# Performance work log

Measured on AMD Instinct MI355X. Metric: run time of the kernel, lower is better.

The kernel has to match this reference:

```python
import jax, jax.numpy as jnp
import numpy as np

D_MODEL = 1024
NHEAD = 16
HEAD_DIM = D_MODEL // NHEAD
D_FF = 4096
EPS = 1e-5


def _layernorm(x, g, b):
    mu = jnp.mean(x, axis=-1, keepdims=True)
    var = jnp.mean(jnp.square(x - mu), axis=-1, keepdims=True)
    return (x - mu) * jax.lax.rsqrt(var + EPS) * g + b


def setup_inputs() -> dict:
    key = jax.random.key(0)
    ks = jax.random.split(key, 8)

    def xavier(k, shape):
        fan_out, fan_in = shape
        lim = np.sqrt(6.0 / (fan_in + fan_out))
        return jax.random.uniform(k, shape, jnp.float32, -lim, lim)

    x = jax.random.normal(ks[0], (4, 2048, D_MODEL), jnp.float32)
    return {
        "x": x,
        "Wq": xavier(ks[1], (D_MODEL, D_MODEL)), "bq": jnp.zeros((D_MODEL,), jnp.float32),
        "Wk": xavier(ks[2], (D_MODEL, D_MODEL)), "bk": jnp.zeros((D_MODEL,), jnp.float32),
        "Wv": xavier(ks[3], (D_MODEL, D_MODEL)), "bv": jnp.zeros((D_MODEL,), jnp.float32),
        "Wo": xavier(ks[4], (D_MODEL, D_MODEL)), "bo": jnp.zeros((D_MODEL,), jnp.float32),
        "W1": xavier(ks[5], (D_FF, D_MODEL)), "b1": jnp.zeros((D_FF,), jnp.float32),
        "W2": xavier(ks[6], (D_MODEL, D_FF)), "b2": jnp.zeros((D_MODEL,), jnp.float32),
        "ln1_g": jnp.ones((D_MODEL,), jnp.float32), "ln1_b": jnp.zeros((D_MODEL,), jnp.float32),
        "ln2_g": jnp.ones((D_MODEL,), jnp.float32), "ln2_b": jnp.zeros((D_MODEL,), jnp.float32),
    }


def reference(x, Wq, bq, Wk, bk, Wv, bv, Wo, bo, W1, b1, W2, b2, ln1_g, ln1_b, ln2_g, ln2_b):
    B, T, D = x.shape
    H, Hd = NHEAD, HEAD_DIM

    # --- attention sublayer (pre-LN) ---
    residual = x
    xn = _layernorm(x, ln1_g, ln1_b)
    # torch Linear: y = x @ W.T + b
    q = (xn @ Wq.T + bq).reshape(B, T, H, Hd).transpose(0, 2, 1, 3)  # [B,H,T,Hd]
    k = (xn @ Wk.T + bk).reshape(B, T, H, Hd).transpose(0, 2, 1, 3)
    v = (xn @ Wv.T + bv).reshape(B, T, H, Hd).transpose(0, 2, 1, 3)

    scale = Hd ** -0.5
    scores = jnp.einsum('bhqd,bhkd->bhqk', q, k) * scale  # [B,H,T,T]
    attn = jax.nn.softmax(scores, axis=-1)
    out = jnp.einsum('bhqk,bhkd->bhqd', attn, v)           # [B,H,T,Hd]
    out = out.transpose(0, 2, 1, 3).reshape(B, T, D)
    out = out @ Wo.T + bo
    x = residual + out

    # --- FFN sublayer (pre-LN) ---
    residual = x
    xn = _layernorm(x, ln2_g, ln2_b)
    h = jax.nn.relu(xn @ W1.T + b1)
    h = h @ W2.T + b2
    return residual + h
```

## Files before the change

kernel.cpp:

```cpp
#include <hip/hip_runtime.h>
#include <hip/hip_bf16.h>

using bf16 = __hip_bfloat16;
typedef __attribute__((ext_vector_type(8))) short bf16x8;
typedef __attribute__((ext_vector_type(4))) float f32x4;

#define D_MODEL 1024
#define NHEAD 16
#define HEAD_DIM 64
#define D_FF 4096
#define SEQ 2048
#define NTOK 8192

__device__ __forceinline__ void gload16(const void* g, void* l) {
  __builtin_amdgcn_global_load_lds((const __attribute__((address_space(1))) void*)g,
                                   (__attribute__((address_space(3))) void*)l, 16, 0, 0);
}

__device__ __forceinline__ unsigned pkbf16(float lo, float hi) {
  unsigned r;
  asm("v_cvt_pk_bf16_f32 %0, %1, %2" : "=v"(r) : "v"(lo), "v"(hi));
  return r;
}

__device__ __forceinline__ float fexp2(float x) {
  float r;
  asm("v_exp_f32 %0, %1" : "=v"(r) : "v"(x));
  return r;
}

__device__ __forceinline__ float max3f(float a, float b, float c) {
  return fmaxf(fmaxf(a, b), c);
}

__global__ __launch_bounds__(256) void cvt_all(
    const float* __restrict__ W1, const float* __restrict__ W2,
    const float* __restrict__ Wq, const float* __restrict__ Wk,
    const float* __restrict__ Wv, const float* __restrict__ Wo,
    bf16* __restrict__ w1_b, bf16* __restrict__ w2_b,
    bf16* __restrict__ wqkv, bf16* __restrict__ wo_b) {
  const int bid = blockIdx.x;
  const float* src;
  bf16* dst;
  int lb;
  if (bid < 4096) { src = W1; dst = w1_b; lb = bid; }
  else if (bid < 8192) { src = W2; dst = w2_b; lb = bid - 4096; }
  else {
    const int j = (bid - 8192) >> 10;
    lb = (bid - 8192) & 1023;
    if (j == 0) { src = Wq; dst = wqkv; }
    else if (j == 1) { src = Wk; dst = wqkv + 1048576; }
    else if (j == 2) { src = Wv; dst = wqkv + 2097152; }
    else { src = Wo; dst = wo_b; }
  }
  const int i = (lb * 256 + threadIdx.x) * 4;
  const float4 v = *(const float4*)&src[i];
  dst[i + 0] = __float2bfloat16(v.x);
  dst[i + 1] = __float2bfloat16(v.y);
  dst[i + 2] = __float2bfloat16(v.z);
  dst[i + 3] = __float2bfloat16(v.w);
}

__global__ __launch_bounds__(256) void layernorm_kernel(
    const float* __restrict__ xin, const float* __restrict__ g,
    const float* __restrict__ bta, bf16* __restrict__ out) {
  const int row = blockIdx.x, t = threadIdx.x;
  const float4 v = *(const float4*)&xin[(size_t)row * D_MODEL + t * 4];
  float s = v.x + v.y + v.z + v.w;
#pragma unroll
  for (int m = 1; m < 64; m <<= 1) s += __shfl_xor(s, m);
  __shared__ float red[4], red2[4];
  const int w = t >> 6, l = t & 63;
  if (l == 0) red[w] = s;
  __syncthreads();
  const float mu = (red[0] + red[1] + red[2] + red[3]) * (1.f / 1024.f);
  const float d0 = v.x - mu, d1 = v.y - mu, d2 = v.z - mu, d3 = v.w - mu;
  float q = d0 * d0 + d1 * d1 + d2 * d2 + d3 * d3;
#pragma unroll
  for (int m = 1; m < 64; m <<= 1) q += __shfl_xor(q, m);
  if (l == 0) red2[w] = q;
  __syncthreads();
  const float var = (red2[0] + red2[1] + red2[2] + red2[3]) * (1.f / 1024.f);
  const float rs = rsqrtf(var + 1e-5f);
  const float4 gg = *(const float4*)&g[t * 4];
  const float4 bb = *(const float4*)&bta[t * 4];
  bf16* o = out + (size_t)row * D_MODEL + t * 4;
  o[0] = __float2bfloat16(d0 * rs * gg.x + bb.x);
  o[1] = __float2bfloat16(d1 * rs * gg.y + bb.y);
  o[2] = __float2bfloat16(d2 * rs * gg.z + bb.z);
  o[3] = __float2bfloat16(d3 * rs * gg.w + bb.w);
}

template <int MODE>
__global__ __launch_bounds__(512, 2) void gemmA(
    const bf16* __restrict__ A, const bf16* __restrict__ Bw,
    const float* __restrict__ bias0, const float* __restrict__ bias1,
    const float* __restrict__ bias2,
    void* __restrict__ out, int M, int N, int K) {
  constexpr int ASZ = 256 * 128;
  constexpr int TILE = ASZ + 256 * 128;
  __shared__ __align__(16) char smem[2 * TILE];

  const int t = threadIdx.x;
  const int l = t & 63, l15 = l & 15, l4 = (l >> 4) & 3;
  const int w = t >> 6, wm = w >> 2, wn = w & 3;
  const int gx = gridDim.x;
  const int nwg = gx * gridDim.y;
  const int bid0 = blockIdx.y * gx + blockIdx.x;
  const int bid = (bid0 & 7) * (nwg >> 3) + (bid0 >> 3);
  const int m0 = (bid / gx) * 256, n0 = (bid % gx) * 256;

  const int sr = t >> 3;
  const int scol = 8 * ((t & 7) ^ (sr & 7));
  const int swz = (l15 & 7) << 4;
  int coff[2];
  coff[0] = (l4 * 16) ^ swz;
  coff[1] = (64 + l4 * 16) ^ swz;

#define ST_A(j, kb, buf)                                          \
  gload16(&A[(size_t)(m0 + (j) * 64 + sr) * K + (kb) + scol],     \
          (void*)(smem + (buf) * TILE + (j) * 8192 + t * 16))
#define ST_B(j, kb, buf)                                          \
  gload16(&Bw[(size_t)(n0 + (j) * 64 + sr) * K + (kb) + scol],    \
          (void*)(smem + (buf) * TILE + ASZ + (j) * 8192 + t * 16))

  f32x4 acc[8][4] = {};
  const int NTm = K >> 6;

  ST_A(0, 0, 0); ST_A(2, 0, 0); ST_B(0, 0, 0);
  ST_B(1, 0, 0); ST_B(2, 0, 0); ST_B(3, 0, 0);
  ST_A(1, 0, 0); ST_A(3, 0, 0);
  asm volatile("s_waitcnt vmcnt(2)" ::: "memory");
  __builtin_amdgcn_s_barrier();

#define PHASE_A(p)                                                                 \
  {                                                                                \
    constexpr int kk = (p) & 1;                                                    \
    constexpr int mh = ((p) >> 1) * 4;                                             \
    bf16x8 af[4], bf[4];                                                           \
    _Pragma("unroll") for (int m = 0; m < 4; ++m)                                  \
      af[m] = *(const bf16x8*)(cb + (wm * 128 + (mh + m) * 16 + l15) * 128 +       \
                               coff[kk]);                                          \
    _Pragma("unroll") for (int n = 0; n < 4; ++n)                                  \
      bf[n] = *(const bf16x8*)(cb + ASZ + (wn * 64 + n * 16 + l15) * 128 +         \
                               coff[kk]);                                          \
    if (hasNext) {                                                                 \
      if ((p) == 0) { ST_A(0, kbn, nb); ST_A(2, kbn, nb); ST_B(0, kbn, nb); }      \
      else if ((p) == 1) { ST_B(1, kbn, nb); ST_B(2, kbn, nb); ST_B(3, kbn, nb); } \
      else if ((p) == 2) { ST_A(1, kbn, nb); ST_A(3, kbn, nb); }                   \
    }                                                                              \
    __builtin_amdgcn_s_barrier();                                                  \
    asm volatile("s_waitcnt lgkmcnt(0)" ::: "memory");                             \
    __builtin_amdgcn_sched_barrier(0);                                             \
    __builtin_amdgcn_s_setprio(1);                                                 \
    _Pragma("unroll") for (int m = 0; m < 4; ++m)                                  \
      _Pragma("unroll") for (int n = 0; n < 4; ++n)                                \
        acc[mh + m][n] = __builtin_amdgcn_mfma_f32_16x16x32_bf16(                  \
            af[m], bf[n], acc[mh + m][n], 0, 0, 0);                                \
    __builtin_amdgcn_s_setprio(0);                                                 \
    if ((p) == 1) {                                                                \
      if (hasNext) asm volatile("s_waitcnt vmcnt(6)" ::: "memory");                \
      else asm volatile("s_waitcnt vmcnt(0)" ::: "memory");                        \
    }                                                                              \
    if ((p) == 3 && hasNext)                                                       \
      asm volatile("s_waitcnt vmcnt(2)" ::: "memory");                             \
    __builtin_amdgcn_s_barrier();                                                  \
  }

  for (int kt = 0; kt < NTm; ++kt) {
    const char* cb = smem + (kt & 1) * TILE;
    const int nb = (kt & 1) ^ 1;
    const int kbn = (kt + 1) << 6;
    const bool hasNext = (kt + 1 < NTm);
    PHASE_A(0) PHASE_A(1) PHASE_A(2) PHASE_A(3)
  }
#undef PHASE_A
#undef ST_A
#undef ST_B

#pragma unroll
  for (int mf = 0; mf < 8; ++mf) {
#pragma unroll
    for (int nf = 0; nf < 4; ++nf) {
      const int col = n0 + wn * 64 + nf * 16 + l15;
      float bb;
      if constexpr (MODE == 0) {
        const int sel = col >> 10;
        const float* bp = (sel == 0) ? bias0 : ((sel == 1) ? bias1 : bias2);
        bb = bp[col & 1023];
      } else {
        bb = bias0[col];
      }
#pragma unroll
      for (int r = 0; r < 4; ++r) {
        const int row = m0 + wm * 128 + mf * 16 + l4 * 4 + r;
        float y = acc[mf][nf][r] + bb;
        if constexpr (MODE == 1) y = fmaxf(y, 0.f);
        if constexpr (MODE == 0) {
          const int sel = col >> 10;
          const int c10 = col & 1023;
          const size_t dst = (size_t)sel * (NTOK * 1024) +
                             (size_t)((row >> 11) * NHEAD + (c10 >> 6)) * (SEQ * HEAD_DIM) +
                             (size_t)(row & (SEQ - 1)) * HEAD_DIM + (c10 & 63);
          ((bf16*)out)[dst] = __float2bfloat16(y);
        } else {
          ((bf16*)out)[(size_t)row * N + col] = __float2bfloat16(y);
        }
      }
    }
  }
}

__global__ __launch_bounds__(512, 2) void gemmB(
    const bf16* __restrict__ A, const bf16* __restrict__ Bw,
    const float* __restrict__ bias, const float* __restrict__ res,
    float* __restrict__ out, int M, int N, int K) {
  constexpr int ASZ = 128 * 128;
  constexpr int TILE = ASZ + 256 * 128;
  __shared__ __align__(16) char smem[3 * TILE];

  const int t = threadIdx.x;
  const int l = t & 63, l15 = l & 15, l4 = (l >> 4) & 3;
  const int w = t >> 6, wm = w >> 2, wn = w & 3;
  const int gx = gridDim.x;
  const int nwg = gx * gridDim.y;
  const int bid0 = blockIdx.y * gx + blockIdx.x;
  const int bid = (bid0 & 7) * (nwg >> 3) + (bid0 >> 3);
  const int m0 = (bid / gx) * 128, n0 = (bid % gx) * 256;

  const int sr = t >> 3;
  const int scol = 8 * ((t & 7) ^ (sr & 7));
  const int swz = (l15 & 7) << 4;
  int coff[2];
  coff[0] = (l4 * 16) ^ swz;
  coff[1] = (64 + l4 * 16) ^ swz;

#define ST_A(j, kb, buf)                                          \
  gload16(&A[(size_t)(m0 + (j) * 64 + sr) * K + (kb) + scol],     \
          (void*)(smem + (buf) * TILE + (j) * 8192 + t * 16))
#define ST_B(j, kb, buf)                                          \
  gload16(&Bw[(size_t)(n0 + (j) * 64 + sr) * K + (kb) + scol],    \
          (void*)(smem + (buf) * TILE + ASZ + (j) * 8192 + t * 16))

  f32x4 acc[4][4] = {};
  const int NTm = K >> 6;

  ST_B(0, 0, 0); ST_B(1, 0, 0); ST_B(2, 0, 0);
  ST_B(3, 0, 0); ST_A(0, 0, 0); ST_A(1, 0, 0);
  ST_B(0, 64, 1); ST_B(1, 64, 1); ST_B(2, 64, 1);
  ST_B(3, 64, 1); ST_A(0, 64, 1); ST_A(1, 64, 1);
  asm volatile("s_waitcnt vmcnt(6)" ::: "memory");
  __builtin_amdgcn_s_barrier();

#define PHASE_B(p)                                                                 \
  {                                                                                \
    constexpr int kk = (p);                                                        \
    bf16x8 af[4], bf[4];                                                           \
    _Pragma("unroll") for (int m = 0; m < 4; ++m)                                  \
      af[m] = *(const bf16x8*)(cb + (wm * 64 + m * 16 + l15) * 128 + coff[kk]);    \
    _Pragma("unroll") for (int n = 0; n < 4; ++n)                                  \
      bf[n] = *(const bf16x8*)(cb + ASZ + (wn * 64 + n * 16 + l15) * 128 +         \
                               coff[kk]);                                          \
    if (iss) {                                                                     \
      if ((p) == 0) { ST_B(0, kbn, nb); ST_B(1, kbn, nb); ST_B(2, kbn, nb); }      \
      else { ST_B(3, kbn, nb); ST_A(0, kbn, nb); ST_A(1, kbn, nb); }               \
    }                                                                              \
    __builtin_amdgcn_s_barrier();                                                  \
    asm volatile("s_waitcnt lgkmcnt(0)" ::: "memory");                             \
    __builtin_amdgcn_sched_barrier(0);                                             \
    __builtin_amdgcn_s_setprio(1);                                                 \
    _Pragma("unroll") for (int m = 0; m < 4; ++m)                                  \
      _Pragma("unroll") for (int n = 0; n < 4; ++n)                                \
        acc[m][n] = __builtin_amdgcn_mfma_f32_16x16x32_bf16(                       \
            af[m], bf[n], acc[m][n], 0, 0, 0);                                     \
    __builtin_amdgcn_s_setprio(0);                                                 \
    if ((p) == 1) {                                                                \
      if (iss) asm volatile("s_waitcnt vmcnt(6)" ::: "memory");                    \
      else asm volatile("s_waitcnt vmcnt(0)" ::: "memory");                        \
    }                                                                              \
    __builtin_amdgcn_s_barrier();                                                  \
  }

  for (int kt = 0; kt < NTm; ++kt) {
    const char* cb = smem + (kt % 3) * TILE;
    const int nb = (kt + 2) % 3;
    const int kbn = (kt + 2) << 6;
    const bool iss = (kt + 2 < NTm);
    PHASE_B(0) PHASE_B(1)
  }
#undef PHASE_B
#undef ST_A
#undef ST_B

#pragma unroll
  for (int mf = 0; mf < 4; ++mf) {
#pragma unroll
    for (int nf = 0; nf < 4; ++nf) {
      const int col = n0 + wn * 64 + nf * 16 + l15;
      const float bb = bias[col];
#pragma unroll
      for (int r = 0; r < 4; ++r) {
        const int row = m0 + wm * 64 + mf * 16 + l4 * 4 + r;
        out[(size_t)row * N + col] = acc[mf][nf][r] + bb + res[(size_t)row * N + col];
      }
    }
  }
}

#define SCL 0.18033688011112042f
#define NT (SEQ / 64)

__global__ __launch_bounds__(512) void flash_attn(
    const bf16* __restrict__ Q, const bf16* __restrict__ K,
    const bf16* __restrict__ V, bf16* __restrict__ O) {
  __shared__ char smem[32768];
  const int t = threadIdx.x;
  const int w = t >> 6, l = t & 63;
  const int l15 = l & 15, l4 = l >> 4;
  const int bid0 = blockIdx.y * 8 + blockIdx.x;
  const int bid = (bid0 & 7) * 64 + (bid0 >> 3);
  const int bx = bid & 7, bh = bid >> 3;
  const size_t base = (size_t)bh * (SEQ * HEAD_DIM);
  const int q0 = bx * 256 + w * 32;

  int krow[4], kswz[4];
#pragma unroll
  for (int ni = 0; ni < 4; ++ni) {
    const int kr = (ni >> 1) * 32 + (ni & 1) * 4 + (l15 >> 2) * 8 + (l15 & 3);
    krow[ni] = kr * 128;
    kswz[ni] = ((kr & 3) | (((kr >> 3) & 1) << 2)) << 4;
  }

  bf16x8 qf[2][2];
#pragma unroll
  for (int mi = 0; mi < 2; ++mi)
#pragma unroll
    for (int kk = 0; kk < 2; ++kk)
      qf[mi][kk] = *(const bf16x8*)&Q[base + (size_t)(q0 + mi * 16 + l15) * 64 + kk * 32 + l4 * 8];

  bf16x8 ones;
#pragma unroll
  for (int j = 0; j < 8; ++j) ones[j] = (short)0x3F80;

  f32x4 accO[2][4] = {};
  float m_run[2], l_run[2];
#pragma unroll
  for (int mi = 0; mi < 2; ++mi) { m_run[mi] = -1e30f; l_run[mi] = 0.f; }

  short vg[8];

  const int r0 = t >> 3;
  const int c0 = 8 * ((t & 7) ^ ((r0 & 3) | (((r0 >> 3) & 1) << 2)));
  const short* kg = (const short*)K + base + r0 * 64 + c0;
  const int dv = t & 63;
  const int kb8 = (t >> 6) * 8;
  const short* vp = (const short*)V + base + (size_t)kb8 * 64 + dv;
  const int vtbyte = dv * 128 + ((kb8 * 2) ^ ((dv & 7) << 4));

#define STAGE_K(bufofs)                                          \
  {                                                              \
    gload16(kg, (void*)(smem + (bufofs) + w * 1024));            \
    kg += 4096;                                                  \
  }

#define V_GATHER()                                               \
  {                                                              \
    _Pragma("unroll") for (int j_ = 0; j_ < 8; ++j_)             \
        vg[j_] = vp[j_ * 64];                                    \
    vp += 4096;                                                  \
  }

#define VT_WRITE(bufofs)                                         \
  {                                                              \
    bf16x8 vv;                                                   \
    _Pragma("unroll") for (int j_ = 0; j_ < 8; ++j_)             \
        vv[j_] = vg[j_];                                         \
    *(bf16x8*)(smem + (bufofs) + vtbyte) = vv;                   \
  }

  STAGE_K(0);
  V_GATHER();
  VT_WRITE(16384);
  __syncthreads();

  for (int it = 0; it < NT; ++it) {
    const int cur = it & 1;
    const char* Kb = (const char*)smem + cur * 8192;
    const char* Vb = (const char*)smem + 16384 + cur * 8192;
    const bool pre = (it + 1 < NT);
    if (pre) {
      STAGE_K((cur ^ 1) * 8192);
      V_GATHER();
    }

    bf16x8 kf[2][4];
#pragma unroll
    for (int kk = 0; kk < 2; ++kk)
#pragma unroll
      for (int ni = 0; ni < 4; ++ni)
        kf[kk][ni] = *(const bf16x8*)(Kb + krow[ni] + ((kk * 64 + l4 * 16) ^ kswz[ni]));

    unsigned pw[2][8];
#pragma unroll
    for (int mi = 0; mi < 2; ++mi) {
      f32x4 s[4] = {};
      __builtin_amdgcn_s_setprio(1);
#pragma unroll
      for (int kk = 0; kk < 2; ++kk)
#pragma unroll
        for (int ni = 0; ni < 4; ++ni)
          s[ni] = __builtin_amdgcn_mfma_f32_16x16x32_bf16(kf[kk][ni], qf[mi][kk], s[ni], 0, 0, 0);
      __builtin_amdgcn_s_setprio(0);

      const float t0 = max3f(s[0][0], s[0][1], s[0][2]);
      const float t1 = max3f(s[0][3], s[1][0], s[1][1]);
      const float t2 = max3f(s[1][2], s[1][3], s[2][0]);
      const float t3 = max3f(s[2][1], s[2][2], s[2][3]);
      const float t4 = max3f(s[3][0], s[3][1], s[3][2]);
      float mx = fmaxf(max3f(t1, t2, t3), fmaxf(t4, fmaxf(t0, s[3][3])));
      mx = fmaxf(mx, __shfl_xor(mx, 16));
      mx = fmaxf(mx, __shfl_xor(mx, 32));
      const float mxs = mx * SCL;
      if (__any(mxs > m_run[mi] + 8.f)) {
        const float mn = fmaxf(m_run[mi], mxs);
        const float c = fexp2(m_run[mi] - mn);
        m_run[mi] = mn;
        l_run[mi] *= c;
#pragma unroll
        for (int ni = 0; ni < 4; ++ni)
#pragma unroll
          for (int r = 0; r < 4; ++r) accO[mi][ni][r] *= c;
      }
#pragma unroll
      for (int ni = 0; ni < 4; ++ni)
#pragma unroll
        for (int r = 0; r < 4; ++r)
          s[ni][r] = fexp2(fmaf(s[ni][r], SCL, -m_run[mi]));
#pragma unroll
      for (int kk = 0; kk < 2; ++kk)
#pragma unroll
        for (int jj = 0; jj < 4; ++jj) {
          const int ni = 2 * kk + (jj >> 1);
          pw[mi][kk * 4 + jj] = pkbf16(s[ni][2 * (jj & 1)], s[ni][2 * (jj & 1) + 1]);
        }
    }

    f32x4 zz[2] = {};
#pragma unroll
    for (int kk = 0; kk < 2; ++kk) {
      bf16x8 vf[4];
#pragma unroll
      for (int ni = 0; ni < 4; ++ni)
        vf[ni] = *(const bf16x8*)(Vb + (ni * 16 + l15) * 128 +
                                  ((kk * 64 + l4 * 16) ^ ((l15 & 7) << 4)));
#pragma unroll
      for (int mi = 0; mi < 2; ++mi) {
        union { unsigned u[4]; bf16x8 h; } pb;
#pragma unroll
        for (int jj = 0; jj < 4; ++jj) pb.u[jj] = pw[mi][kk * 4 + jj];
        __builtin_amdgcn_s_setprio(1);
#pragma unroll
        for (int ni = 0; ni < 4; ++ni)
          accO[mi][ni] = __builtin_amdgcn_mfma_f32_16x16x32_bf16(vf[ni], pb.h, accO[mi][ni], 0, 0, 0);
        zz[mi] = __builtin_amdgcn_mfma_f32_16x16x32_bf16(ones, pb.h, zz[mi], 0, 0, 0);
        __builtin_amdgcn_s_setprio(0);
      }
    }
#pragma unroll
    for (int mi = 0; mi < 2; ++mi) l_run[mi] += zz[mi][0];

    if (pre) VT_WRITE(16384 + (cur ^ 1) * 8192);
    __syncthreads();
  }

  char* ob = smem + w * 4096;
#pragma unroll
  for (int mi = 0; mi < 2; ++mi) {
    const float inv = 1.f / l_run[mi];
    const int qr = mi * 16 + l15;
    const int sw = (qr & 7) << 4;
#pragma unroll
    for (int ni = 0; ni < 4; ++ni)
#pragma unroll
      for (int rr = 0; rr < 2; ++rr) {
        const unsigned pk = pkbf16(accO[mi][ni][2 * rr] * inv, accO[mi][ni][2 * rr + 1] * inv);
        *(unsigned*)(ob + qr * 128 + ((ni * 32 + l4 * 8 + 4 * rr) ^ sw)) = pk;
      }
  }
  asm volatile("s_waitcnt lgkmcnt(0)" ::: "memory");
  __builtin_amdgcn_sched_barrier(0);

  const int b = bh >> 4, h = bh & 15;
  const int hr = l >> 1, hf = l & 1;
  const size_t orow = ((size_t)b * SEQ + bx * 256 + w * 32 + hr) * D_MODEL + h * HEAD_DIM + hf * 32;
#pragma unroll
  for (int c = 0; c < 4; ++c) {
    bf16x8 vv = *(const bf16x8*)(ob + hr * 128 + (((hf * 64) + c * 16) ^ ((hr & 7) << 4)));
    *(bf16x8*)&O[orow + c * 8] = vv;
  }
}

extern "C" void kernel_launch(void* const* d_in, const int* in_sizes, int n_in,
                              void* d_out, int out_size, void* d_ws, size_t ws_size,
                              hipStream_t stream) {
  const float* x     = (const float*)d_in[0];
  const float* Wq    = (const float*)d_in[1];
  const float* bq    = (const float*)d_in[2];
  const float* Wk    = (const float*)d_in[3];
  const float* bk    = (const float*)d_in[4];
  const float* Wv    = (const float*)d_in[5];
  const float* bv    = (const float*)d_in[6];
  const float* Wo    = (const float*)d_in[7];
  const float* bo    = (const float*)d_in[8];
  const float* W1    = (const float*)d_in[9];
  const float* b1    = (const float*)d_in[10];
  const float* W2    = (const float*)d_in[11];
  const float* b2    = (const float*)d_in[12];
  const float* ln1_g = (const float*)d_in[13];
  const float* ln1_b = (const float*)d_in[14];
  const float* ln2_g = (const float*)d_in[15];
  const float* ln2_b = (const float*)d_in[16];

  const size_t MB = 1ull << 20;
  char* ws = (char*)d_ws;
  bf16* wqkv = (bf16*)(ws + 0 * MB);
  bf16* wo_b = (bf16*)(ws + 6 * MB);
  bf16* w1_b = (bf16*)(ws + 8 * MB);
  bf16* w2_b = (bf16*)(ws + 16 * MB);
  bf16* xn   = (bf16*)(ws + 24 * MB);
  bf16* qb   = (bf16*)(ws + 40 * MB);
  bf16* kbuf = (bf16*)(ws + 56 * MB);
  bf16* vb   = (bf16*)(ws + 72 * MB);
  bf16* hb   = (bf16*)(ws + 40 * MB);
  float* x1  = (float*)(ws + 104 * MB);

  cvt_all<<<12288, 256, 0, stream>>>(W1, W2, Wq, Wk, Wv, Wo, w1_b, w2_b, wqkv, wo_b);

  layernorm_kernel<<<NTOK, 256, 0, stream>>>(x, ln1_g, ln1_b, xn);

  gemmA<0><<<dim3(3072 / 256, NTOK / 256), 512, 0, stream>>>(
      xn, wqkv, bq, bk, bv, qb, NTOK, 3072, 1024);

  flash_attn<<<dim3(SEQ / 256, 4 * NHEAD), 512, 0, stream>>>(qb, kbuf, vb, xn);

  gemmB<<<dim3(1024 / 256, NTOK / 128), 512, 0, stream>>>(
      xn, wo_b, bo, x, x1, NTOK, 1024, 1024);

  layernorm_kernel<<<NTOK, 256, 0, stream>>>(x1, ln2_g, ln2_b, xn);

  gemmA<1><<<dim3(D_FF / 256, NTOK / 256), 512, 0, stream>>>(
      xn, w1_b, b1, b1, b1, hb, NTOK, D_FF, 1024);

  gemmB<<<dim3(1024 / 256, NTOK / 128), 512, 0, stream>>>(
      hb, w2_b, b2, x1, (float*)d_out, NTOK, 1024, D_FF);
}
```

Baseline: 384.4 us.

## Simplify GEMM pipelines and move QKV projection onto 128-row triple-buffered kernel

Both GEMM kernels drop the fine-grained four-phase and two-phase schedules, which interleaved async loads with barriers and partial vmcnt waits. The new loops issue each tile's loads up front, read all fragments, run the MFMAs, then do one wait and one barrier per k-step. The QKV projection moves from the 256x256 double-buffered kernel to the 128x256 triple-buffered kernel, now templated to handle the head-split scatter output. gemmA keeps only the FFN1 path and now waits on vmcnt(0) every iteration, which may expose load latency. The changes aim to cut barrier and sync overhead and to raise the QKV grid size, at the cost of less overlap between loads and compute.

```diff
diff --git a/kernel.cpp b/kernel.cpp
--- a/kernel.cpp
+++ b/kernel.cpp
@@ -94,8 +94,7 @@
 template <int MODE>
 __global__ __launch_bounds__(512, 2) void gemmA(
     const bf16* __restrict__ A, const bf16* __restrict__ Bw,
-    const float* __restrict__ bias0, const float* __restrict__ bias1,
-    const float* __restrict__ bias2,
+    const float* __restrict__ bias0,
     void* __restrict__ out, int M, int N, int K) {
   constexpr int ASZ = 256 * 128;
   constexpr int TILE = ASZ + 256 * 128;
@@ -127,59 +126,142 @@
   f32x4 acc[8][4] = {};
   const int NTm = K >> 6;
 
-  ST_A(0, 0, 0); ST_A(2, 0, 0); ST_B(0, 0, 0);
-  ST_B(1, 0, 0); ST_B(2, 0, 0); ST_B(3, 0, 0);
-  ST_A(1, 0, 0); ST_A(3, 0, 0);
-  asm volatile("s_waitcnt vmcnt(2)" ::: "memory");
+  ST_A(0, 0, 0); ST_A(2, 0, 0); ST_B(0, 0, 0); ST_B(1, 0, 0);
+  ST_B(2, 0, 0); ST_B(3, 0, 0); ST_A(1, 0, 0); ST_A(3, 0, 0);
+  asm volatile("s_waitcnt vmcnt(0)" ::: "memory");
   __builtin_amdgcn_s_barrier();
-
-#define PHASE_A(p)                                                                 \
-  {                                                                                \
-    constexpr int kk = (p) & 1;                                                    \
-    constexpr int mh = ((p) >> 1) * 4;                                             \
-    bf16x8 af[4], bf[4];                                                           \
-    _Pragma("unroll") for (int m = 0; m < 4; ++m)                                  \
-      af[m] = *(const bf16x8*)(cb + (wm * 128 + (mh + m) * 16 + l15) * 128 +       \
-                               coff[kk]);                                          \
-    _Pragma("unroll") for (int n = 0; n < 4; ++n)                                  \
-      bf[n] = *(const bf16x8*)(cb + ASZ + (wn * 64 + n * 16 + l15) * 128 +         \
-                               coff[kk]);                                          \
-    if (hasNext) {                                                                 \
-      if ((p) == 0) { ST_A(0, kbn, nb); ST_A(2, kbn, nb); ST_B(0, kbn, nb); }      \
-      else if ((p) == 1) { ST_B(1, kbn, nb); ST_B(2, kbn, nb); ST_B(3, kbn, nb); } \
-      else if ((p) == 2) { ST_A(1, kbn, nb); ST_A(3, kbn, nb); }                   \
-    }                                                                              \
-    __builtin_amdgcn_s_barrier();                                                  \
-    asm volatile("s_waitcnt lgkmcnt(0)" ::: "memory");                             \
-    __builtin_amdgcn_sched_barrier(0);                                             \
-    __builtin_amdgcn_s_setprio(1);                                                 \
-    _Pragma("unroll") for (int m = 0; m < 4; ++m)                                  \
-      _Pragma("unroll") for (int n = 0; n < 4; ++n)                                \
-        acc[mh + m][n] = __builtin_amdgcn_mfma_f32_16x16x32_bf16(                  \
-            af[m], bf[n], acc[mh + m][n], 0, 0, 0);                                \
-    __builtin_amdgcn_s_setprio(0);                                                 \
-    if ((p) == 1) {                                                                \
-      if (hasNext) asm volatile("s_waitcnt vmcnt(6)" ::: "memory");                \
-      else asm volatile("s_waitcnt vmcnt(0)" ::: "memory");                        \
-    }                                                                              \
-    if ((p) == 3 && hasNext)                                                       \
-      asm volatile("s_waitcnt vmcnt(2)" ::: "memory");                             \
-    __builtin_amdgcn_s_barrier();                                                  \
-  }
 
   for (int kt = 0; kt < NTm; ++kt) {
     const char* cb = smem + (kt & 1) * TILE;
     const int nb = (kt & 1) ^ 1;
     const int kbn = (kt + 1) << 6;
     const bool hasNext = (kt + 1 < NTm);
-    PHASE_A(0) PHASE_A(1) PHASE_A(2) PHASE_A(3)
-  }
-#undef PHASE_A
+#pragma unroll
+    for (int kk = 0; kk < 2; ++kk) {
+      if (hasNext) {
+        if (kk == 0) { ST_A(0, kbn, nb); ST_A(2, kbn, nb); ST_B(0, kbn, nb); ST_B(1, kbn, nb); }
+        else         { ST_B(2, kbn, nb); ST_B(3, kbn, nb); ST_A(1, kbn, nb); ST_A(3, kbn, nb); }
+      }
+      bf16x8 af[8], bfr[4];
+#pragma unroll
+      for (int mf = 0; mf < 8; ++mf)
+        af[mf] = *(const bf16x8*)(cb + (wm * 128 + mf * 16 + l15) * 128 + coff[kk]);
+#pragma unroll
+      for (int nf = 0; nf < 4; ++nf)
+        bfr[nf] = *(const bf16x8*)(cb + ASZ + (wn * 64 + nf * 16 + l15) * 128 + coff[kk]);
+      __builtin_amdgcn_s_setprio(1);
+#pragma unroll
+      for (int mf = 0; mf < 8; ++mf)
+#pragma unroll
+        for (int nf = 0; nf < 4; ++nf)
+          acc[mf][nf] = __builtin_amdgcn_mfma_f32_16x16x32_bf16(
+              af[mf], bfr[nf], acc[mf][nf], 0, 0, 0);
+      __builtin_amdgcn_s_setprio(0);
+    }
+    asm volatile("s_waitcnt vmcnt(0)" ::: "memory");
+    __builtin_amdgcn_s_barrier();
+  }
 #undef ST_A
 #undef ST_B
 
 #pragma unroll
   for (int mf = 0; mf < 8; ++mf) {
+#pragma unroll
+    for (int nf = 0; nf < 4; ++nf) {
+      const int col = n0 + wn * 64 + nf * 16 + l15;
+      const float bb = bias0[col];
+#pragma unroll
+      for (int r = 0; r < 4; ++r) {
+        const int row = m0 + wm * 128 + mf * 16 + l4 * 4 + r;
+        float y = acc[mf][nf][r] + bb;
+        if constexpr (MODE == 1) y = fmaxf(y, 0.f);
+        ((bf16*)out)[(size_t)row * N + col] = __float2bfloat16(y);
+      }
+    }
+  }
+}
+
+template <int MODE>
+__global__ __launch_bounds__(512, 2) void gemmB(
+    const bf16* __restrict__ A, const bf16* __restrict__ Bw,
+    const float* __restrict__ bias0, const float* __restrict__ bias1,
+    const float* __restrict__ bias2, const float* __restrict__ res,
+    void* __restrict__ out, int M, int N, int K) {
+  constexpr int ASZ = 128 * 128;
+  constexpr int TILE = ASZ + 256 * 128;
+  __shared__ __align__(16) char smem[3 * TILE];
+
+  const int t = threadIdx.x;
+  const int l = t & 63, l15 = l & 15, l4 = (l >> 4) & 3;
+  const int w = t >> 6, wm = w >> 2, wn = w & 3;
+  const int gx = gridDim.x;
+  const int nwg = gx * gridDim.y;
+  const int bid0 = blockIdx.y * gx + blockIdx.x;
+  const int bid = (bid0 & 7) * (nwg >> 3) + (bid0 >> 3);
+  const int m0 = (bid / gx) * 128, n0 = (bid % gx) * 256;
+
+  const int sr = t >> 3;
+  const int scol = 8 * ((t & 7) ^ (sr & 7));
+  const int swz = (l15 & 7) << 4;
+  int coff[2];
+  coff[0] = (l4 * 16) ^ swz;
+  coff[1] = (64 + l4 * 16) ^ swz;
+
+#define ST_A(j, kb, buf)                                          \
+  gload16(&A[(size_t)(m0 + (j) * 64 + sr) * K + (kb) + scol],     \
+          (void*)(smem + (buf) * TILE + (j) * 8192 + t * 16))
+#define ST_B(j, kb, buf)                                          \
+  gload16(&Bw[(size_t)(n0 + (j) * 64 + sr) * K + (kb) + scol],    \
+          (void*)(smem + (buf) * TILE + ASZ + (j) * 8192 + t * 16))
+
+  f32x4 acc[4][4] = {};
+  const int NTm = K >> 6;
+
+  ST_B(0, 0, 0); ST_B(1, 0, 0); ST_B(2, 0, 0);
+  ST_B(3, 0, 0); ST_A(0, 0, 0); ST_A(1, 0, 0);
+  ST_B(0, 64, 1); ST_B(1, 64, 1); ST_B(2, 64, 1);
+  ST_B(3, 64, 1); ST_A(0, 64, 1); ST_A(1, 64, 1);
+  asm volatile("s_waitcnt vmcnt(6)" ::: "memory");
+  __builtin_amdgcn_s_barrier();
+
+  for (int kt = 0; kt < NTm; ++kt) {
+    const char* cb = smem + (kt % 3) * TILE;
+    const int nb = (kt + 2) % 3;
+    const int kbn = (kt + 2) << 6;
+    const bool iss = (kt + 2 < NTm);
+    if (iss) {
+      ST_B(0, kbn, nb); ST_B(1, kbn, nb); ST_B(2, kbn, nb);
+      ST_B(3, kbn, nb); ST_A(0, kbn, nb); ST_A(1, kbn, nb);
+    }
+    bf16x8 af[2][4], bfr[2][4];
+#pragma unroll
+    for (int kk = 0; kk < 2; ++kk) {
+#pragma unroll
+      for (int mf = 0; mf < 4; ++mf)
+        af[kk][mf] = *(const bf16x8*)(cb + (wm * 64 + mf * 16 + l15) * 128 + coff[kk]);
+#pragma unroll
+      for (int nf = 0; nf < 4; ++nf)
+        bfr[kk][nf] = *(const bf16x8*)(cb + ASZ + (wn * 64 + nf * 16 + l15) * 128 + coff[kk]);
+    }
+    __builtin_amdgcn_s_setprio(1);
+#pragma unroll
+    for (int kk = 0; kk < 2; ++kk)
+#pragma unroll
+      for (int mf = 0; mf < 4; ++mf)
+#pragma unroll
+        for (int nf = 0; nf < 4; ++nf)
+          acc[mf][nf] = __builtin_amdgcn_mfma_f32_16x16x32_bf16(
+              af[kk][mf], bfr[kk][nf], acc[mf][nf], 0, 0, 0);
+    __builtin_amdgcn_s_setprio(0);
+    if (iss) asm volatile("s_waitcnt vmcnt(6)" ::: "memory");
+    else     asm volatile("s_waitcnt vmcnt(0)" ::: "memory");
+    __builtin_amdgcn_s_barrier();
+  }
+#undef ST_A
+#undef ST_B
+
+#pragma unroll
+  for (int mf = 0; mf < 4; ++mf) {
 #pragma unroll
     for (int nf = 0; nf < 4; ++nf) {
       const int col = n0 + wn * 64 + nf * 16 + l15;
@@ -193,9 +275,8 @@
       }
 #pragma unroll
       for (int r = 0; r < 4; ++r) {
-        const int row = m0 + wm * 128 + mf * 16 + l4 * 4 + r;
+        const int row = m0 + wm * 64 + mf * 16 + l4 * 4 + r;
         float y = acc[mf][nf][r] + bb;
-        if constexpr (MODE == 1) y = fmaxf(y, 0.f);
         if constexpr (MODE == 0) {
           const int sel = col >> 10;
           const int c10 = col & 1023;
@@ -204,104 +285,9 @@
                              (size_t)(row & (SEQ - 1)) * HEAD_DIM + (c10 & 63);
           ((bf16*)out)[dst] = __float2bfloat16(y);
         } else {
-          ((bf16*)out)[(size_t)row * N + col] = __float2bfloat16(y);
+          y += res[(size_t)row * N + col];
+          ((float*)out)[(size_t)row * N + col] = y;
         }
-      }
-    }
-  }
-}
-
-__global__ __launch_bounds__(512, 2) void gemmB(
-    const bf16* __restrict__ A, const bf16* __restrict__ Bw,
-    const float* __restrict__ bias, const float* __restrict__ res,
-    float* __restrict__ out, int M, int N, int K) {
-  constexpr int ASZ = 128 * 128;
-  constexpr int TILE = ASZ + 256 * 128;
-  __shared__ __align__(16) char smem[3 * TILE];
-
-  const int t = threadIdx.x;
-  const int l = t & 63, l15 = l & 15, l4 = (l >> 4) & 3;
-  const int w = t >> 6, wm = w >> 2, wn = w & 3;
-  const int gx = gridDim.x;
-  const int nwg = gx * gridDim.y;
-  const int bid0 = blockIdx.y * gx + blockIdx.x;
-  const int bid = (bid0 & 7) * (nwg >> 3) + (bid0 >> 3);
-  const int m0 = (bid / gx) * 128, n0 = (bid % gx) * 256;
-
-  const int sr = t >> 3;
-  const int scol = 8 * ((t & 7) ^ (sr & 7));
-  const int swz = (l15 & 7) << 4;
-  int coff[2];
-  coff[0] = (l4 * 16) ^ swz;
-  coff[1] = (64 + l4 * 16) ^ swz;
-
-#define ST_A(j, kb, buf)                                          \
-  gload16(&A[(size_t)(m0 + (j) * 64 + sr) * K + (kb) + scol],     \
-          (void*)(smem + (buf) * TILE + (j) * 8192 + t * 16))
-#define ST_B(j, kb, buf)                                          \
-  gload16(&Bw[(size_t)(n0 + (j) * 64 + sr) * K + (kb) + scol],    \
-          (void*)(smem + (buf) * TILE + ASZ + (j) * 8192 + t * 16))
-
-  f32x4 acc[4][4] = {};
-  const int NTm = K >> 6;
-
-  ST_B(0, 0, 0); ST_B(1, 0, 0); ST_B(2, 0, 0);
-  ST_B(3, 0, 0); ST_A(0, 0, 0); ST_A(1, 0, 0);
-  ST_B(0, 64, 1); ST_B(1, 64, 1); ST_B(2, 64, 1);
-  ST_B(3, 64, 1); ST_A(0, 64, 1); ST_A(1, 64, 1);
-  asm volatile("s_waitcnt vmcnt(6)" ::: "memory");
-  __builtin_amdgcn_s_barrier();
-
-#define PHASE_B(p)                                                                 \
-  {                                                                                \
-    constexpr int kk = (p);                                                        \
-    bf16x8 af[4], bf[4];                                                           \
-    _Pragma("unroll") for (int m = 0; m < 4; ++m)                                  \
-      af[m] = *(const bf16x8*)(cb + (wm * 64 + m * 16 + l15) * 128 + coff[kk]);    \
-    _Pragma("unroll") for (int n = 0; n < 4; ++n)                                  \
-      bf[n] = *(const bf16x8*)(cb + ASZ + (wn * 64 + n * 16 + l15) * 128 +         \
-                               coff[kk]);                                          \
-    if (iss) {                                                                     \
-      if ((p) == 0) { ST_B(0, kbn, nb); ST_B(1, kbn, nb); ST_B(2, kbn, nb); }      \
-      else { ST_B(3, kbn, nb); ST_A(0, kbn, nb); ST_A(1, kbn, nb); }               \
-    }                                                                              \
-    __builtin_amdgcn_s_barrier();                                                  \
-    asm volatile("s_waitcnt lgkmcnt(0)" ::: "memory");                             \
-    __builtin_amdgcn_sched_barrier(0);                                             \
-    __builtin_amdgcn_s_setprio(1);                                                 \
-    _Pragma("unroll") for (int m = 0; m < 4; ++m)                                  \
-      _Pragma("unroll") for (int n = 0; n < 4; ++n)                                \
-        acc[m][n] = __builtin_amdgcn_mfma_f32_16x16x32_bf16(                       \
-            af[m], bf[n], acc[m][n], 0, 0, 0);                                     \
-    __builtin_amdgcn_s_setprio(0);                                                 \
-    if ((p) == 1) {                                                                \
-      if (iss) asm volatile("s_waitcnt vmcnt(6)" ::: "memory");                    \
-      else asm volatile("s_waitcnt vmcnt(0)" ::: "memory");                        \
-    }                                                                              \
-    __builtin_amdgcn_s_barrier();                                                  \
-  }
-
-  for (int kt = 0; kt < NTm; ++kt) {
-    const char* cb = smem + (kt % 3) * TILE;
-    const int nb = (kt + 2) % 3;
-    const int kbn = (kt + 2) << 6;
-    const bool iss = (kt + 2 < NTm);
-    PHASE_B(0) PHASE_B(1)
-  }
-#undef PHASE_B
-#undef ST_A
-#undef ST_B
-
-#pragma unroll
-  for (int mf = 0; mf < 4; ++mf) {
-#pragma unroll
-    for (int nf = 0; nf < 4; ++nf) {
-      const int col = n0 + wn * 64 + nf * 16 + l15;
-      const float bb = bias[col];
-#pragma unroll
-      for (int r = 0; r < 4; ++r) {
-        const int row = m0 + wm * 64 + mf * 16 + l4 * 4 + r;
-        out[(size_t)row * N + col] = acc[mf][nf][r] + bb + res[(size_t)row * N + col];
       }
     }
   }
@@ -538,19 +524,19 @@
 
   layernorm_kernel<<<NTOK, 256, 0, stream>>>(x, ln1_g, ln1_b, xn);
 
-  gemmA<0><<<dim3(3072 / 256, NTOK / 256), 512, 0, stream>>>(
-      xn, wqkv, bq, bk, bv, qb, NTOK, 3072, 1024);
+  gemmB<0><<<dim3(3072 / 256, NTOK / 128), 512, 0, stream>>>(
+      xn, wqkv, bq, bk, bv, nullptr, qb, NTOK, 3072, 1024);
 
   flash_attn<<<dim3(SEQ / 256, 4 * NHEAD), 512, 0, stream>>>(qb, kbuf, vb, xn);
 
-  gemmB<<<dim3(1024 / 256, NTOK / 128), 512, 0, stream>>>(
-      xn, wo_b, bo, x, x1, NTOK, 1024, 1024);
+  gemmB<2><<<dim3(1024 / 256, NTOK / 128), 512, 0, stream>>>(
+      xn, wo_b, bo, bo, bo, x, x1, NTOK, 1024, 1024);
 
   layernorm_kernel<<<NTOK, 256, 0, stream>>>(x1, ln2_g, ln2_b, xn);
 
   gemmA<1><<<dim3(D_FF / 256, NTOK / 256), 512, 0, stream>>>(
-      xn, w1_b, b1, b1, b1, hb, NTOK, D_FF, 1024);
-
-  gemmB<<<dim3(1024 / 256, NTOK / 128), 512, 0, stream>>>(
-      hb, w2_b, b2, x1, (float*)d_out, NTOK, 1024, D_FF);
-}
+      xn, w1_b, b1, hb, NTOK, D_FF, 1024);
+
+  gemmB<2><<<dim3(1024 / 256, NTOK / 128), 512, 0, stream>>>(
+      hb, w2_b, b2, b2, b2, x1, d_out, NTOK, 1024, D_FF);
+}
```

Result: no change. 382.1 us (-0.6%).
